# Performance work log

Measured on AMD Instinct MI355X. Metric: run time of the kernel, lower is better.

Reference implementation:

```python
import jax, jax.numpy as jnp
import numpy as np
from jax import lax


def _conv2d_same(x, w, b):
    # NHWC input, HWIO kernel, stride 1, SAME padding (matches keras Conv2D)
    y = lax.conv_general_dilated(x, w, window_strides=(1, 1), padding='SAME',
                                 dimension_numbers=('NHWC', 'HWIO', 'NHWC'))
    return y + b


def setup_inputs() -> dict:
    key = jax.random.key(0)
    k1, k2, k3, k4 = jax.random.split(key, 4)
    B, H, W, C = 16, 128, 128, 256
    F = 256
    inputs = jax.random.normal(k1, (B, H, W, C), dtype=jnp.float32)
    # offset conv: small random weights so offsets are non-trivial but in-range-ish
    w_off = jax.random.normal(k2, (3, 3, C, 2), dtype=jnp.float32) * 0.05
    b_off = jnp.zeros((2,), dtype=jnp.float32)
    w_def = jax.random.normal(k3, (3, 3, C, F), dtype=jnp.float32) * (1.0 / np.sqrt(9 * C))
    b_def = jax.random.normal(k4, (F,), dtype=jnp.float32) * 0.01
    return {"inputs": inputs, "w_off": w_off, "b_off": b_off,
            "w_def": w_def, "b_def": b_def}


def reference(inputs, w_off, b_off, w_def, b_def):
    B, H, W, C = inputs.shape
    # 1) predict per-pixel (dy, dx) offsets
    offsets = _conv2d_same(inputs, w_off, b_off)          # (B,H,W,2)
    off_h = offsets[..., 0]                               # (B,H,W)
    off_w = offsets[..., 1]                               # (B,H,W)
    # 2) build sampling grid, add offsets, clip, truncate to int (tf.cast semantics;
    #    values are non-negative after clip so truncation == floor)
    yy, xx = jnp.meshgrid(jnp.arange(H, dtype=inputs.dtype),
                          jnp.arange(W, dtype=inputs.dtype), indexing='ij')
    y = jnp.clip(yy[None] + off_h, 0.0, H - 1).astype(jnp.int32)   # (B,H,W)
    x = jnp.clip(xx[None] + off_w, 0.0, W - 1).astype(jnp.int32)   # (B,H,W)
    # 3) gather: one offset per pixel, shared across all channels
    lin = (y * W + x).reshape(B, H * W, 1)                # (B,HW,1)
    sampled = jnp.take_along_axis(inputs.reshape(B, H * W, C), lin, axis=1)
    sampled = sampled.reshape(B, H, W, C)
    # 4) main conv on resampled features
    return _conv2d_same(sampled, w_def, b_def)
```

## Files before the change

### kernel.cpp

```cpp
#include <hip/hip_runtime.h>
#include <hip/hip_bf16.h>

typedef __attribute__((ext_vector_type(8))) short bf16x8;
typedef __attribute__((ext_vector_type(4))) float f32x4;

__device__ __forceinline__ unsigned short f2bf(float f) {
  __hip_bfloat16 h = __float2bfloat16(f);
  return *reinterpret_cast<unsigned short*>(&h);
}

__device__ __forceinline__ void gld_lds16(void* lds, const void* g) {
  __builtin_amdgcn_global_load_lds(
      (const __attribute__((address_space(1))) unsigned int*)g,
      (__attribute__((address_space(3))) unsigned int*)lds, 16, 0, 0);
}

__global__ __launch_bounds__(256) void k1_offs_gather(
    const float* __restrict__ in, const float* __restrict__ w_off,
    const float* __restrict__ b_off, unsigned short* __restrict__ samp) {
  __shared__ float tile[3][128][34];
  __shared__ float wlf[9 * 64];
  __shared__ double dsum[2][128][2];
  __shared__ int lin_lds[128];

  const int bid = blockIdx.x;
  const int b = bid >> 7, h = bid & 127;
  const int t = threadIdx.x;
  const int w = t & 127, half = t >> 7, ch0 = half * 16;

  double a0 = 0.0, a1 = 0.0;

  for (int c0 = 0; c0 < 256; c0 += 32) {
    __syncthreads();
    for (int i = t; i < 576; i += 256) {
      int tap = i >> 6, r = i & 63;
      wlf[i] = w_off[tap * 512 + c0 * 2 + r];
    }
    for (int dr = 0; dr < 3; ++dr) {
      int hh = h + dr - 1;
      if ((unsigned)hh < 128u) {
        const float* rbase = in + ((size_t)(b * 128 + hh) * 128) * 256 + c0;
        #pragma unroll
        for (int it = 0; it < 4; ++it) {
          int idx = it * 256 + t;
          int ww = idx >> 3, cq = idx & 7;
          const float4 v = *(const float4*)(rbase + ww * 256 + cq * 4);
          float* dst = &tile[dr][ww][cq * 4];
          *(float2*)dst = make_float2(v.x, v.y);
          *(float2*)(dst + 2) = make_float2(v.z, v.w);
        }
      } else {
        #pragma unroll
        for (int it = 0; it < 4; ++it) {
          int idx = it * 256 + t;
          int ww = idx >> 3, cq = idx & 7;
          float* dst = &tile[dr][ww][cq * 4];
          *(float2*)dst = make_float2(0.f, 0.f);
          *(float2*)(dst + 2) = make_float2(0.f, 0.f);
        }
      }
    }
    __syncthreads();
    #pragma unroll
    for (int dr = 0; dr < 3; ++dr) {
      #pragma unroll
      for (int dc = 0; dc < 3; ++dc) {
        int wsrc = w + dc - 1;
        if ((unsigned)wsrc >= 128u) continue;
        const float2* tp2 = (const float2*)&tile[dr][wsrc][ch0];
        const float2* wp2 = (const float2*)&wlf[(dr * 3 + dc) * 64 + ch0 * 2];
        #pragma unroll
        for (int c2 = 0; c2 < 8; ++c2) {
          float2 v = tp2[c2];
          float2 wa = wp2[2 * c2];
          float2 wb = wp2[2 * c2 + 1];
          a0 += (double)v.x * (double)wa.x;
          a1 += (double)v.x * (double)wa.y;
          a0 += (double)v.y * (double)wb.x;
          a1 += (double)v.y * (double)wb.y;
        }
      }
    }
  }
  dsum[half][w][0] = a0;
  dsum[half][w][1] = a1;
  __syncthreads();
  if (t < 128) {
    double o0 = dsum[0][t][0] + dsum[1][t][0] + (double)b_off[0];
    double o1 = dsum[0][t][1] + dsum[1][t][1] + (double)b_off[1];
    double yd = (double)h + o0;
    double xd = (double)t + o1;
    yd = yd < 0.0 ? 0.0 : (yd > 127.0 ? 127.0 : yd);
    xd = xd < 0.0 ? 0.0 : (xd > 127.0 ? 127.0 : xd);
    int y = (int)yd, x = (int)xd;
    lin_lds[t] = y * 128 + x;
  }
  __syncthreads();
  const float* imgbase = in + (size_t)b * 16384 * 256;
  unsigned short* obase = samp + (size_t)bid * 128 * 256;
  for (int it = 0; it < 32; ++it) {
    int idx = it * 256 + t;
    int px = idx >> 6, cv = idx & 63;
    const float4 v = *(const float4*)(imgbase + (size_t)lin_lds[px] * 256 + cv * 4);
    ushort4 o;
    o.x = f2bf(v.x); o.y = f2bf(v.y); o.z = f2bf(v.z); o.w = f2bf(v.w);
    *(ushort4*)(obase + px * 256 + cv * 4) = o;
  }
}

__global__ __launch_bounds__(256) void k2_wT(const float* __restrict__ wdef,
                                             unsigned short* __restrict__ wT) {
  int g = blockIdx.x * 256 + threadIdx.x;
  int tap = g >> 16;
  int n = (g >> 8) & 255;
  int k = g & 255;
  wT[g] = f2bf(wdef[((size_t)tap * 256 + k) * 256 + n]);
}

__global__ __launch_bounds__(512, 2) void k3_conv(
    const unsigned short* __restrict__ samp, const unsigned short* __restrict__ wT,
    const float* __restrict__ b_def, float* __restrict__ out,
    const unsigned short* __restrict__ zerobuf) {
  __shared__ __align__(16) unsigned char smem[131072];

  const int bid0 = blockIdx.x;
  const int mt = (bid0 & 7) * 128 + (bid0 >> 3);
  const int bimg = mt >> 6;
  const int h0 = (mt & 63) * 2;

  const int tid = threadIdx.x;
  const int lane = tid & 63, wave = tid >> 6;
  const int wr = wave >> 2, wc = wave & 3;
  const int r15 = lane & 15, g4 = lane >> 4;
  const int g4eff = g4 ^ ((r15 >> 1) & 3);

  int aoff[8], boff[4];
  #pragma unroll
  for (int mi = 0; mi < 8; ++mi)
    aoff[mi] = (wr * 128 + mi * 16 + r15) * 32 + g4eff * 8;
  #pragma unroll
  for (int ni = 0; ni < 4; ++ni)
    boff[ni] = (wc * 64 + ni * 16 + r15) * 32 + g4eff * 8;

  const int chq = tid & 3;
  const int pix = tid >> 2;
  const int chs = chq ^ ((pix >> 1) & 3);
  const unsigned short* pA[2];
  const unsigned short* pB[2];
  unsigned vmask[2];
  #pragma unroll
  for (int it = 0; it < 2; ++it) {
    const int hh = h0 + it;
    pA[it] = samp + ((size_t)(bimg * 128 + hh) * 128 + pix) * 256 + chs * 8;
    pB[it] = wT + (size_t)(it * 128 + pix) * 256 + chs * 8;
    unsigned m = 0;
    #pragma unroll
    for (int tap = 0; tap < 9; ++tap) {
      const int dr = tap / 3 - 1, dc = tap % 3 - 1;
      if ((unsigned)(hh + dr) < 128u && (unsigned)(pix + dc) < 128u)
        m |= 1u << tap;
    }
    vmask[it] = m;
  }
  const unsigned short* zb = zerobuf + chq * 8;

  f32x4 acc[8][4];
  #pragma unroll
  for (int i = 0; i < 8; ++i)
    #pragma unroll
    for (int j = 0; j < 4; ++j) acc[i][j] = (f32x4){0.f, 0.f, 0.f, 0.f};

  auto stage = [&](int ts) {
    const int tap = ts >> 3, kc = ts & 7;
    const int q = (tap * 11) >> 5;
    const int tapdelta = ((q - 1) * 128 + (tap - q * 3 - 1)) * 256 + kc * 32;
    const int boffg = tap * 65536 + kc * 32;
    unsigned char* Ad = smem + (size_t)(ts & 3) * 16384;
    unsigned char* Bd = smem + 65536 + (size_t)(ts & 3) * 16384;
    #pragma unroll
    for (int it = 0; it < 2; ++it)
      gld_lds16(Bd + (it * 512 + tid) * 16, pB[it] + boffg);
    #pragma unroll
    for (int it = 0; it < 2; ++it) {
      const unsigned short* src =
          ((vmask[it] >> tap) & 1) ? (pA[it] + tapdelta) : zb;
      gld_lds16(Ad + (it * 512 + tid) * 16, src);
    }
  };

  auto readfrags = [&](int T, bf16x8* af, bf16x8* bfr) {
    const unsigned short* Ab = (const unsigned short*)(smem + (size_t)(T & 3) * 16384);
    const unsigned short* Bb = (const unsigned short*)(smem + 65536 + (size_t)(T & 3) * 16384);
    #pragma unroll
    for (int ni = 0; ni < 4; ++ni) bfr[ni] = *(const bf16x8*)(Bb + boff[ni]);
    #pragma unroll
    for (int mi = 0; mi < 8; ++mi) af[mi] = *(const bf16x8*)(Ab + aoff[mi]);
  };

  auto mfma32 = [&](bf16x8* af, bf16x8* bfr) {
    __builtin_amdgcn_s_setprio(1);
    #pragma unroll
    for (int mi = 0; mi < 8; ++mi)
      #pragma unroll
      for (int ni = 0; ni < 4; ++ni)
        acc[mi][ni] = __builtin_amdgcn_mfma_f32_16x16x32_bf16(
            af[mi], bfr[ni], acc[mi][ni], 0, 0, 0);
    __builtin_amdgcn_s_setprio(0);
  };

  stage(0); stage(1); stage(2);
  asm volatile("s_waitcnt vmcnt(8)" ::: "memory");
  __builtin_amdgcn_s_barrier();
  asm volatile("" ::: "memory");
  __builtin_amdgcn_sched_barrier(0);

  for (int t = 0; t < 69; ++t) {
    bf16x8 af[8], bfr[4];
    readfrags(t, af, bfr);
    stage(t + 3);
    __builtin_amdgcn_sched_barrier(0);
    mfma32(af, bfr);
    asm volatile("s_waitcnt vmcnt(8)" ::: "memory");
    __builtin_amdgcn_s_barrier();
    asm volatile("" ::: "memory");
    __builtin_amdgcn_sched_barrier(0);
  }
  {
    bf16x8 af[8], bfr[4];
    readfrags(69, af, bfr);
    __builtin_amdgcn_sched_barrier(0);
    mfma32(af, bfr);
    asm volatile("s_waitcnt vmcnt(4)" ::: "memory");
    __builtin_amdgcn_s_barrier();
    asm volatile("" ::: "memory");
    __builtin_amdgcn_sched_barrier(0);
  }
  {
    bf16x8 af[8], bfr[4];
    readfrags(70, af, bfr);
    __builtin_amdgcn_sched_barrier(0);
    mfma32(af, bfr);
    asm volatile("s_waitcnt vmcnt(0)" ::: "memory");
    __builtin_amdgcn_s_barrier();
    asm volatile("" ::: "memory");
    __builtin_amdgcn_sched_barrier(0);
  }
  {
    bf16x8 af[8], bfr[4];
    readfrags(71, af, bfr);
    __builtin_amdgcn_sched_barrier(0);
    mfma32(af, bfr);
  }

  const int colg = wc * 64 + r15;
  float bias[4];
  #pragma unroll
  for (int ni = 0; ni < 4; ++ni) bias[ni] = b_def[colg + ni * 16];
  #pragma unroll
  for (int mi = 0; mi < 8; ++mi) {
    const int r0 = wr * 128 + mi * 16 + g4 * 4;
    #pragma unroll
    for (int j = 0; j < 4; ++j) {
      float* orow = out + ((size_t)mt * 256 + r0 + j) * 256 + colg;
      #pragma unroll
      for (int ni = 0; ni < 4; ++ni) orow[ni * 16] = acc[mi][ni][j] + bias[ni];
    }
  }
}

extern "C" void kernel_launch(void* const* d_in, const int* in_sizes, int n_in,
                              void* d_out, int out_size, void* d_ws, size_t ws_size,
                              hipStream_t stream) {
  const float* in = (const float*)d_in[0];
  const float* w_off = (const float*)d_in[1];
  const float* b_off = (const float*)d_in[2];
  const float* w_def = (const float*)d_in[3];
  const float* b_def = (const float*)d_in[4];
  float* out = (float*)d_out;

  char* ws = (char*)d_ws;
  unsigned short* zerobuf = (unsigned short*)ws;
  unsigned short* wT = (unsigned short*)(ws + 4096);
  unsigned short* samp = (unsigned short*)(ws + 4096 + 1179648);

  hipMemsetAsync(ws, 0, 4096, stream);
  hipLaunchKernelGGL(k2_wT, dim3(2304), dim3(256), 0, stream, w_def, wT);
  hipLaunchKernelGGL(k1_offs_gather, dim3(2048), dim3(256), 0, stream,
                     in, w_off, b_off, samp);
  hipLaunchKernelGGL(k3_conv, dim3(1024), dim3(512), 0, stream,
                     samp, wT, b_def, out, zerobuf);
}
```

Before: 508.3 us.

## Split conv main loop into two half-phases with extra barriers for ping-pong overlap

Each K-step of the deformable conv GEMM is split into two halves: read B fragments plus half of the A fragments, barrier, run half the MFMAs, barrier, then read the remaining A fragments and issue the next global->LDS stage before the second MFMA half. The goal is to interleave LDS reads and global loads with MFMA work across waves, in the style of a ping-pong schedule, and to cut register pressure from holding all fragments at once. It adds four barriers per step and removes the sched_barrier hints. Stage issue now happens after the first half's MFMAs rather than before them.

```diff
diff --git a/kernel.cpp b/kernel.cpp
--- a/kernel.cpp
+++ b/kernel.cpp
@@ -188,69 +188,72 @@
     }
   };
 
-  auto readfrags = [&](int T, bf16x8* af, bf16x8* bfr) {
+  auto readsA = [&](int T, bf16x8* af, bf16x8* fb) {
     const unsigned short* Ab = (const unsigned short*)(smem + (size_t)(T & 3) * 16384);
     const unsigned short* Bb = (const unsigned short*)(smem + 65536 + (size_t)(T & 3) * 16384);
     #pragma unroll
-    for (int ni = 0; ni < 4; ++ni) bfr[ni] = *(const bf16x8*)(Bb + boff[ni]);
-    #pragma unroll
-    for (int mi = 0; mi < 8; ++mi) af[mi] = *(const bf16x8*)(Ab + aoff[mi]);
-  };
-
-  auto mfma32 = [&](bf16x8* af, bf16x8* bfr) {
+    for (int ni = 0; ni < 4; ++ni) fb[ni] = *(const bf16x8*)(Bb + boff[ni]);
+    #pragma unroll
+    for (int mi = 0; mi < 4; ++mi) af[mi] = *(const bf16x8*)(Ab + aoff[mi]);
+  };
+  auto readsB = [&](int T, bf16x8* af) {
+    const unsigned short* Ab = (const unsigned short*)(smem + (size_t)(T & 3) * 16384);
+    #pragma unroll
+    for (int mi = 4; mi < 8; ++mi) af[mi] = *(const bf16x8*)(Ab + aoff[mi]);
+  };
+  auto mfmaA = [&](bf16x8* af, bf16x8* fb) {
     __builtin_amdgcn_s_setprio(1);
     #pragma unroll
-    for (int mi = 0; mi < 8; ++mi)
+    for (int mi = 0; mi < 4; ++mi)
       #pragma unroll
       for (int ni = 0; ni < 4; ++ni)
         acc[mi][ni] = __builtin_amdgcn_mfma_f32_16x16x32_bf16(
-            af[mi], bfr[ni], acc[mi][ni], 0, 0, 0);
+            af[mi], fb[ni], acc[mi][ni], 0, 0, 0);
     __builtin_amdgcn_s_setprio(0);
   };
+  auto mfmaB = [&](bf16x8* af, bf16x8* fb) {
+    __builtin_amdgcn_s_setprio(1);
+    #pragma unroll
+    for (int mi = 4; mi < 8; ++mi)
+      #pragma unroll
+      for (int ni = 0; ni < 4; ++ni)
+        acc[mi][ni] = __builtin_amdgcn_mfma_f32_16x16x32_bf16(
+            af[mi], fb[ni], acc[mi][ni], 0, 0, 0);
+    __builtin_amdgcn_s_setprio(0);
+  };
+
+#define K3_STEP(T, VM, DO_STAGE)                            \
+  {                                                         \
+    bf16x8 af[8], fb[4];                                    \
+    readsA(T, af, fb);                                      \
+    asm volatile("" ::: "memory");                          \
+    __builtin_amdgcn_s_barrier();                           \
+    asm volatile("" ::: "memory");                          \
+    mfmaA(af, fb);                                          \
+    asm volatile("" ::: "memory");                          \
+    __builtin_amdgcn_s_barrier();                           \
+    asm volatile("" ::: "memory");                          \
+    readsB(T, af);                                          \
+    if (DO_STAGE) stage((T) + 3);                           \
+    asm volatile("s_waitcnt vmcnt(" #VM ")" ::: "memory");  \
+    __builtin_amdgcn_s_barrier();                           \
+    asm volatile("" ::: "memory");                          \
+    mfmaB(af, fb);                                          \
+    asm volatile("" ::: "memory");                          \
+    __builtin_amdgcn_s_barrier();                           \
+    asm volatile("" ::: "memory");                          \
+  }
 
   stage(0); stage(1); stage(2);
   asm volatile("s_waitcnt vmcnt(8)" ::: "memory");
   __builtin_amdgcn_s_barrier();
   asm volatile("" ::: "memory");
-  __builtin_amdgcn_sched_barrier(0);
-
-  for (int t = 0; t < 69; ++t) {
-    bf16x8 af[8], bfr[4];
-    readfrags(t, af, bfr);
-    stage(t + 3);
-    __builtin_amdgcn_sched_barrier(0);
-    mfma32(af, bfr);
-    asm volatile("s_waitcnt vmcnt(8)" ::: "memory");
-    __builtin_amdgcn_s_barrier();
-    asm volatile("" ::: "memory");
-    __builtin_amdgcn_sched_barrier(0);
-  }
-  {
-    bf16x8 af[8], bfr[4];
-    readfrags(69, af, bfr);
-    __builtin_amdgcn_sched_barrier(0);
-    mfma32(af, bfr);
-    asm volatile("s_waitcnt vmcnt(4)" ::: "memory");
-    __builtin_amdgcn_s_barrier();
-    asm volatile("" ::: "memory");
-    __builtin_amdgcn_sched_barrier(0);
-  }
-  {
-    bf16x8 af[8], bfr[4];
-    readfrags(70, af, bfr);
-    __builtin_amdgcn_sched_barrier(0);
-    mfma32(af, bfr);
-    asm volatile("s_waitcnt vmcnt(0)" ::: "memory");
-    __builtin_amdgcn_s_barrier();
-    asm volatile("" ::: "memory");
-    __builtin_amdgcn_sched_barrier(0);
-  }
-  {
-    bf16x8 af[8], bfr[4];
-    readfrags(71, af, bfr);
-    __builtin_amdgcn_sched_barrier(0);
-    mfma32(af, bfr);
-  }
+
+  for (int t = 0; t < 69; ++t) K3_STEP(t, 8, true);
+  K3_STEP(69, 4, false);
+  K3_STEP(70, 0, false);
+  K3_STEP(71, 0, false);
+#undef K3_STEP
 
   const int colg = wc * 64 + r15;
   float bias[4];
```

New measurement: 528.4 us. 4.0% more time.

## Double-buffer MFMA fragments and interleave LDS reads with MFMAs in conv main loop

Applied to the files above, without the earlier changes.

Restructures the conv kernel's main loop so the LDS fragment reads for the next k-step are issued during the MFMAs of the current step, using two register fragment sets and sched_group_barrier to interleave MFMA, DS-read and global-load-to-LDS instructions. The loop is unrolled by four with compile-time slot indices, and LDS addresses become constant offsets from precomputed base pointers. The vmcnt waits are adjusted to the new pipeline depth. This aims to hide LDS read latency behind matrix math, at the cost of more vector registers for the second fragment set, which could pressure occupancy at 2 blocks of 512 threads.

```diff
diff --git a/kernel.cpp b/kernel.cpp
--- a/kernel.cpp
+++ b/kernel.cpp
@@ -117,6 +117,8 @@
   wT[g] = f2bf(wdef[((size_t)tap * 256 + k) * 256 + n]);
 }
 
+struct Frags { bf16x8 a[8]; bf16x8 b[4]; };
+
 __global__ __launch_bounds__(512, 2) void k3_conv(
     const unsigned short* __restrict__ samp, const unsigned short* __restrict__ wT,
     const float* __restrict__ b_def, float* __restrict__ out,
@@ -134,13 +136,8 @@
   const int r15 = lane & 15, g4 = lane >> 4;
   const int g4eff = g4 ^ ((r15 >> 1) & 3);
 
-  int aoff[8], boff[4];
-  #pragma unroll
-  for (int mi = 0; mi < 8; ++mi)
-    aoff[mi] = (wr * 128 + mi * 16 + r15) * 32 + g4eff * 8;
-  #pragma unroll
-  for (int ni = 0; ni < 4; ++ni)
-    boff[ni] = (wc * 64 + ni * 16 + r15) * 32 + g4eff * 8;
+  const char* sA = (const char*)smem + (wr * 128 + r15) * 64 + g4eff * 16;
+  const char* sB = (const char*)smem + 65536 + (wc * 64 + r15) * 64 + g4eff * 16;
 
   const int chq = tid & 3;
   const int pix = tid >> 2;
@@ -170,13 +167,13 @@
     #pragma unroll
     for (int j = 0; j < 4; ++j) acc[i][j] = (f32x4){0.f, 0.f, 0.f, 0.f};
 
-  auto stage = [&](int ts) {
+  auto stage = [&](int ts, int SLOT) {
     const int tap = ts >> 3, kc = ts & 7;
     const int q = (tap * 11) >> 5;
     const int tapdelta = ((q - 1) * 128 + (tap - q * 3 - 1)) * 256 + kc * 32;
     const int boffg = tap * 65536 + kc * 32;
-    unsigned char* Ad = smem + (size_t)(ts & 3) * 16384;
-    unsigned char* Bd = smem + 65536 + (size_t)(ts & 3) * 16384;
+    unsigned char* Ad = smem + SLOT * 16384;
+    unsigned char* Bd = smem + 65536 + SLOT * 16384;
     #pragma unroll
     for (int it = 0; it < 2; ++it)
       gld_lds16(Bd + (it * 512 + tid) * 16, pB[it] + boffg);
@@ -188,69 +185,79 @@
     }
   };
 
-  auto readfrags = [&](int T, bf16x8* af, bf16x8* bfr) {
-    const unsigned short* Ab = (const unsigned short*)(smem + (size_t)(T & 3) * 16384);
-    const unsigned short* Bb = (const unsigned short*)(smem + 65536 + (size_t)(T & 3) * 16384);
-    #pragma unroll
-    for (int ni = 0; ni < 4; ++ni) bfr[ni] = *(const bf16x8*)(Bb + boff[ni]);
-    #pragma unroll
-    for (int mi = 0; mi < 8; ++mi) af[mi] = *(const bf16x8*)(Ab + aoff[mi]);
-  };
-
-  auto mfma32 = [&](bf16x8* af, bf16x8* bfr) {
-    __builtin_amdgcn_s_setprio(1);
+  auto readfr = [&](Frags& f, int SLOT) {
+    #pragma unroll
+    for (int ni = 0; ni < 4; ++ni)
+      f.b[ni] = *(const bf16x8*)(sB + SLOT * 16384 + ni * 1024);
+    #pragma unroll
+    for (int mi = 0; mi < 8; ++mi)
+      f.a[mi] = *(const bf16x8*)(sA + SLOT * 16384 + mi * 1024);
+  };
+
+  auto launder = [&](Frags& f) {
+    #pragma unroll
+    for (int i = 0; i < 8; ++i) asm volatile("" : "+v"(f.a[i]));
+    #pragma unroll
+    for (int i = 0; i < 4; ++i) asm volatile("" : "+v"(f.b[i]));
+  };
+
+  auto mfma32 = [&](Frags& f) {
     #pragma unroll
     for (int mi = 0; mi < 8; ++mi)
       #pragma unroll
       for (int ni = 0; ni < 4; ++ni)
         acc[mi][ni] = __builtin_amdgcn_mfma_f32_16x16x32_bf16(
-            af[mi], bfr[ni], acc[mi][ni], 0, 0, 0);
-    __builtin_amdgcn_s_setprio(0);
-  };
-
-  stage(0); stage(1); stage(2);
-  asm volatile("s_waitcnt vmcnt(8)" ::: "memory");
+            f.a[mi], f.b[ni], acc[mi][ni], 0, 0, 0);
+  };
+
+  Frags fr0, fr1;
+
+#define K3_STEP(T_RT, SLOT_NXT, FR_CUR, FR_NXT, DO_READS, DO_STAGE, VMSTR) \
+  {                                                                        \
+    asm volatile("s_waitcnt lgkmcnt(0)" ::: "memory");                     \
+    launder(FR_CUR);                                                       \
+    __builtin_amdgcn_sched_barrier(0);                                     \
+    __builtin_amdgcn_s_setprio(1);                                         \
+    if (DO_READS) readfr(FR_NXT, SLOT_NXT);                                \
+    if (DO_STAGE) stage((T_RT) + 3, ((SLOT_NXT) + 2) & 3);                 \
+    mfma32(FR_CUR);                                                        \
+    if (DO_READS && DO_STAGE) {                                            \
+      _Pragma("unroll")                                                    \
+      for (int u = 0; u < 4; ++u) {                                        \
+        __builtin_amdgcn_sched_group_barrier(0x008, 8, 0);                 \
+        __builtin_amdgcn_sched_group_barrier(0x100, 3, 0);                 \
+        __builtin_amdgcn_sched_group_barrier(0x030, 1, 0);                 \
+      }                                                                    \
+    }                                                                      \
+    __builtin_amdgcn_s_setprio(0);                                         \
+    __builtin_amdgcn_sched_barrier(0);                                     \
+    asm volatile("s_waitcnt " VMSTR ::: "memory");                         \
+    __builtin_amdgcn_s_barrier();                                          \
+    asm volatile("" ::: "memory");                                         \
+  }
+
+  stage(0, 0); stage(1, 1); stage(2, 2);
+  asm volatile("s_waitcnt vmcnt(4)" ::: "memory");
   __builtin_amdgcn_s_barrier();
   asm volatile("" ::: "memory");
-  __builtin_amdgcn_sched_barrier(0);
-
-  for (int t = 0; t < 69; ++t) {
-    bf16x8 af[8], bfr[4];
-    readfrags(t, af, bfr);
-    stage(t + 3);
+  readfr(fr0, 0);
+
+  for (int tb = 0; tb < 68; tb += 4) {
+    K3_STEP(tb + 0, 1, fr0, fr1, true, true, "vmcnt(4)");
+    K3_STEP(tb + 1, 2, fr1, fr0, true, true, "vmcnt(4)");
+    K3_STEP(tb + 2, 3, fr0, fr1, true, true, "vmcnt(4)");
+    K3_STEP(tb + 3, 0, fr1, fr0, true, true, "vmcnt(4)");
+  }
+  K3_STEP(68, 1, fr0, fr1, true, true,  "vmcnt(4)");
+  K3_STEP(69, 2, fr1, fr0, true, false, "vmcnt(0)");
+  K3_STEP(70, 3, fr0, fr1, true, false, "vmcnt(0)");
+  {
+    asm volatile("s_waitcnt lgkmcnt(0)" ::: "memory");
+    launder(fr1);
     __builtin_amdgcn_sched_barrier(0);
-    mfma32(af, bfr);
-    asm volatile("s_waitcnt vmcnt(8)" ::: "memory");
-    __builtin_amdgcn_s_barrier();
-    asm volatile("" ::: "memory");
-    __builtin_amdgcn_sched_barrier(0);
-  }
-  {
-    bf16x8 af[8], bfr[4];
-    readfrags(69, af, bfr);
-    __builtin_amdgcn_sched_barrier(0);
-    mfma32(af, bfr);
-    asm volatile("s_waitcnt vmcnt(4)" ::: "memory");
-    __builtin_amdgcn_s_barrier();
-    asm volatile("" ::: "memory");
-    __builtin_amdgcn_sched_barrier(0);
-  }
-  {
-    bf16x8 af[8], bfr[4];
-    readfrags(70, af, bfr);
-    __builtin_amdgcn_sched_barrier(0);
-    mfma32(af, bfr);
-    asm volatile("s_waitcnt vmcnt(0)" ::: "memory");
-    __builtin_amdgcn_s_barrier();
-    asm volatile("" ::: "memory");
-    __builtin_amdgcn_sched_barrier(0);
-  }
-  {
-    bf16x8 af[8], bfr[4];
-    readfrags(71, af, bfr);
-    __builtin_amdgcn_sched_barrier(0);
-    mfma32(af, bfr);
-  }
+    mfma32(fr1);
+  }
+#undef K3_STEP
 
   const int colg = wc * 64 + r15;
   float bias[4];
```

Result: faster. 492.7 us (-3.1%).
